# Kernel tuning notes

Measured on AMD Instinct MI355X. Metric: run time of the kernel, lower is better.

Reference implementation:

```python
import jax, jax.numpy as jnp
import numpy as np

TEMP = 0.1
LAM = 1.0
NORM_EPS = 1e-12   # torch F.normalize eps
COS_EPS = 1e-8     # torch F.cosine_similarity eps


def l2norm(x, axis):
    n = jnp.sqrt(jnp.sum(x * x, axis=axis, keepdims=True))
    return x / jnp.maximum(n, NORM_EPS)


def cos_sim(a, b, axis):
    na = jnp.sqrt(jnp.sum(a * a, axis=axis))
    nb = jnp.sqrt(jnp.sum(b * b, axis=axis))
    return jnp.sum(a * b, axis=axis) / jnp.maximum(na * nb, COS_EPS)


def setup_inputs() -> dict:
    key = jax.random.key(0)
    k1, k2, k3, k4, k5 = jax.random.split(key, 5)
    B, C, H, W = 32, 256, 32, 32
    return {
        "q_b": jax.random.normal(k1, (B, C, H, W), dtype=jnp.float32),
        "k_b": jax.random.normal(k2, (B, C, H, W), dtype=jnp.float32),
        "q_grid": jax.random.normal(k3, (B, C, H, W), dtype=jnp.float32),
        "k_grid": jax.random.normal(k4, (B, C, H, W), dtype=jnp.float32),
        "labels": jax.random.randint(k5, (B,), 0, 10, dtype=jnp.int64),
    }


def densecl(q_b, k_b, q_grid, k_grid, labels):
    B, C, H, W = q_b.shape
    S = H * W
    q_b = l2norm(q_b, axis=1)
    k_b = l2norm(k_b, axis=1)
    q_grid = l2norm(q_grid, axis=1)
    k_grid = l2norm(k_grid, axis=1)

    q_b_flat = q_b.reshape(B, C, S)
    k_b_flat = k_b.reshape(B, C, S)
    # spatial correspondence: [B, S, S]
    sim = jnp.einsum('bci,bcj->bij', q_b_flat, k_b_flat)
    max_sim_idx = jnp.argmax(sim, axis=-1)  # [B, S]

    Cg = q_grid.shape[1]
    q_grid_flat = q_grid.reshape(B, Cg, S)
    k_grid_flat = k_grid.reshape(B, Cg, S)
    idx = jnp.broadcast_to(max_sim_idx[:, None, :], (B, Cg, S))
    k_matched = jnp.take_along_axis(k_grid_flat, idx, axis=2)
    pos_sim = cos_sim(q_grid_flat, k_matched, axis=1) / TEMP  # [B, S]

    # random negative from a different-label sample (use_prototypes=False path)
    key = jax.random.key(42)
    u = jax.random.uniform(key, (B, B))
    mask = labels[:, None] != labels[None, :]
    neg_idx = jnp.argmax(jnp.where(mask, u, -1.0), axis=1)  # [B]
    neg_k = k_grid_flat[neg_idx]  # [B, Cg, S]
    neg_sim = cos_sim(q_grid_flat, neg_k, axis=1) / TEMP  # [B, S]

    loss = -jnp.log(jnp.exp(pos_sim) / (jnp.exp(pos_sim) + jnp.exp(neg_sim) + 1e-6))
    return jnp.mean(loss)


def reference(q_b, k_b, q_grid, k_grid, labels):
    return densecl(q_b, k_b, q_grid, k_grid, labels) * LAM
```

## Files before the change

kernel.cpp:

```cpp
#include <hip/hip_runtime.h>
#include <hip/hip_bf16.h>
#include <math.h>
#include <stdint.h>

#define BB 32
#define CC 256
#define SS 1024

typedef __attribute__((ext_vector_type(8))) short short8v;
typedef __attribute__((ext_vector_type(4))) float f32x4;

#define ASYNC16(g, l)                                                        \
  __builtin_amdgcn_global_load_lds(                                          \
      (const __attribute__((address_space(1))) void*)(g),                    \
      (__attribute__((address_space(3))) void*)(l), 16, 0, 0)

__device__ __forceinline__ unsigned short bf16_rne(float f) {
  unsigned int u = __float_as_uint(f);
  unsigned int r = (u + 0x7fffu + ((u >> 16) & 1u)) >> 16;
  return (unsigned short)r;
}

__device__ __forceinline__ void tf_round(uint32_t& x0, uint32_t& x1, int r) {
  x0 += x1;
  x1 = (x1 << r) | (x1 >> (32 - r));
  x1 ^= x0;
}

__device__ __forceinline__ void tf_gen(int t, float* u) {
  uint32_t x0 = (uint32_t)t;
  uint32_t x1 = (uint32_t)(t + 512);
  const uint32_t ks0 = 0u, ks1 = 42u, ks2 = 0x1BD11BDAu ^ 0u ^ 42u;
  x0 += ks0; x1 += ks1;
  tf_round(x0, x1, 13); tf_round(x0, x1, 15); tf_round(x0, x1, 26); tf_round(x0, x1, 6);
  x0 += ks1; x1 += ks2 + 1u;
  tf_round(x0, x1, 17); tf_round(x0, x1, 29); tf_round(x0, x1, 16); tf_round(x0, x1, 24);
  x0 += ks2; x1 += ks0 + 2u;
  tf_round(x0, x1, 13); tf_round(x0, x1, 15); tf_round(x0, x1, 26); tf_round(x0, x1, 6);
  x0 += ks0; x1 += ks1 + 3u;
  tf_round(x0, x1, 17); tf_round(x0, x1, 29); tf_round(x0, x1, 16); tf_round(x0, x1, 24);
  x0 += ks1; x1 += ks2 + 4u;
  tf_round(x0, x1, 13); tf_round(x0, x1, 15); tf_round(x0, x1, 26); tf_round(x0, x1, 6);
  x0 += ks2; x1 += ks0 + 5u;
  u[t]       = __uint_as_float((x0 >> 9) | 0x3f800000u) - 1.0f;
  u[t + 512] = __uint_as_float((x1 >> 9) | 0x3f800000u) - 1.0f;
}

__device__ __forceinline__ void tn_body(const float* __restrict__ src,
                                        unsigned short* __restrict__ dst,
                                        float* __restrict__ inv, int b, int s0,
                                        int tid, unsigned int* tile,
                                        float (*part)[65]) {
  const int sg = tid & 15;
  const int cq = tid >> 4;

  const float* sp = src + (size_t)b * CC * SS + s0 + sg * 4;
  float ssq[4] = {0.f, 0.f, 0.f, 0.f};

#pragma unroll
  for (int half = 0; half < 2; ++half) {
    float4 xa[4], xb[4];
#pragma unroll
    for (int kk = 0; kk < 4; ++kk) {
      int cp = cq + 16 * (half * 4 + kk);
      int c = cp * 2;
      xa[kk] = *(const float4*)(sp + ((size_t)c << 10));
      xb[kk] = *(const float4*)(sp + ((size_t)(c + 1) << 10));
    }
#pragma unroll
    for (int kk = 0; kk < 4; ++kk) {
      int cp = cq + 16 * (half * 4 + kk);
      float a[4] = {xa[kk].x, xa[kk].y, xa[kk].z, xa[kk].w};
      float bb[4] = {xb[kk].x, xb[kk].y, xb[kk].z, xb[kk].w};
#pragma unroll
      for (int e = 0; e < 4; ++e) {
        ssq[e] = fmaf(a[e], a[e], ssq[e]);
        ssq[e] = fmaf(bb[e], bb[e], ssq[e]);
        int r = sg * 4 + e;
        int colp = cp ^ (sg << 2);
        tile[r * 128 + colp] =
            (unsigned)bf16_rne(a[e]) | ((unsigned)bf16_rne(bb[e]) << 16);
      }
    }
  }
#pragma unroll
  for (int e = 0; e < 4; ++e) part[cq][sg * 4 + e] = ssq[e];
  __syncthreads();

  const int h = tid >> 5, cw = tid & 31;
  unsigned short* dp = dst + ((size_t)b * SS + s0) * CC;
#pragma unroll
  for (int p = 0; p < 8; ++p) {
    int r = p * 8 + h;
    int colb = (cw * 4) ^ ((r >> 2) << 2);
    uint4 pk = *(const uint4*)&tile[r * 128 + colb];
    *(uint4*)(dp + (size_t)r * CC + cw * 8) = pk;
  }
  if (tid < 64) {
    float s = 0.f;
#pragma unroll
    for (int k = 0; k < 16; ++k) s += part[k][tid];
    inv[b * SS + s0 + tid] = 1.0f / fmaxf(sqrtf(s), 1e-12f);
  }
}

__global__ __launch_bounds__(256, 4) void transnorm_kernel(
    const float* __restrict__ qb, const float* __restrict__ kb,
    unsigned short* __restrict__ qt, unsigned short* __restrict__ kt,
    float* __restrict__ invqb, float* __restrict__ invkb,
    const int* __restrict__ labels, int* __restrict__ negidx,
    unsigned long long* __restrict__ best, float* __restrict__ out) {
  const int bid = blockIdx.x;
  const int tid = threadIdx.x;

  __shared__ unsigned int tile[64 * 128];
  __shared__ float part[16][65];

  if (bid >= 1024) {
    if (bid == 1024) {
      float* u = (float*)&tile[0];
      tf_gen(tid, u);
      tf_gen(tid + 256, u);
      if (tid == 0) *out = 0.f;
      __syncthreads();
      if (tid < BB) {
        int lb = labels[tid];
        float bestv = -1.0f;
        int bj = 0;
        for (int j = 0; j < BB; ++j) {
          float v = (labels[j] != lb) ? u[tid * BB + j] : -1.0f;
          if (v > bestv) { bestv = v; bj = j; }
        }
        negidx[tid] = bj;
      }
    } else {
      unsigned long long* bp = best + (size_t)(bid - 1025) * 8192 + tid;
#pragma unroll
      for (int i = 0; i < 32; ++i) bp[(size_t)i * 256] = 0ull;
    }
    return;
  }

  const int which = bid >> 9;
  const int sub = bid & 511;
  tn_body(which ? kb : qb, which ? kt : qt, which ? invkb : invqb, sub >> 4,
          (sub & 15) * 64, tid, tile, part);
}

__device__ __forceinline__ void sim_stage(
    const unsigned short* __restrict__ aG, const unsigned short* __restrict__ bG,
    unsigned short* SA, unsigned short* SB, int ch, int w, int r8, int p) {
#pragma unroll
  for (int v = 0; v < 4; ++v) {
    int r = v * 32 + w * 8 + r8;
    int clog = p ^ (r & 7);
    ASYNC16(aG + (size_t)r * CC + ch * 64 + clog * 8, &SA[(v * 32 + w * 8) * 64]);
    ASYNC16(bG + (size_t)r * CC + ch * 64 + clog * 8, &SB[(v * 32 + w * 8) * 64]);
  }
}

__device__ __forceinline__ void sim_compute(
    const unsigned short* SA, const unsigned short* SB, f32x4 acc[4][4],
    int wi, int wj, int q4, int m16) {
#pragma unroll
  for (int kk = 0; kk < 2; ++kk) {
    short8v af[4], bf[4];
#pragma unroll
    for (int mt = 0; mt < 4; ++mt) {
      int i = wi + mt * 16 + m16;
      int cp = (kk * 4 + q4) ^ (i & 7);
      af[mt] = *(const short8v*)&SA[i * 64 + cp * 8];
      int j = wj + mt * 16 + m16;
      int cq = (kk * 4 + q4) ^ (j & 7);
      bf[mt] = *(const short8v*)&SB[j * 64 + cq * 8];
    }
#pragma unroll
    for (int mt = 0; mt < 4; ++mt)
#pragma unroll
      for (int nt = 0; nt < 4; ++nt)
        acc[mt][nt] = __builtin_amdgcn_mfma_f32_16x16x32_bf16(
            af[mt], bf[nt], acc[mt][nt], 0, 0, 0);
  }
}

__global__ __launch_bounds__(256, 2) void megasim_kernel(
    const unsigned short* __restrict__ qt, const unsigned short* __restrict__ kt,
    const float* __restrict__ invk, unsigned long long* __restrict__ best,
    const float* __restrict__ kg, unsigned short* __restrict__ kgt,
    float* __restrict__ invkg) {
  __shared__ __align__(16) char smem[68096];
  const int bid = blockIdx.x;
  const int t = threadIdx.x;

  if ((bid % 5) == 4) {
    const int tn_idx = bid / 5;
    tn_body(kg, kgt, invkg, tn_idx >> 4, (tn_idx & 15) * 64, t,
            (unsigned int*)smem, (float(*)[65])(smem + 32768));
    return;
  }

  const int x = bid & 7;
  const int k = ((bid % 40) - x) >> 3;
  int o = 0;
#pragma unroll
  for (int kk = 0; kk < 4; ++kk)
    if (kk < k && ((x + 8 * kk) % 5) != 4) ++o;
  const int W = x * 256 + (bid / 40) * 4 + o;
  const int b = W >> 6, it = (W >> 3) & 7, jt = W & 7;
  const int w = t >> 6, l = t & 63;

  unsigned short* sa0 = (unsigned short*)(smem);
  unsigned short* sa1 = (unsigned short*)(smem + 16384);
  unsigned short* sb0 = (unsigned short*)(smem + 32768);
  unsigned short* sb1 = (unsigned short*)(smem + 49152);
  unsigned long long (*cand2)[2] = (unsigned long long(*)[2])(smem + 65536);
  float* sinvk = (float*)(smem + 65536 + 2048);

  if (t < 128) sinvk[t] = invk[b * SS + jt * 128 + t];

  const unsigned short* aG = qt + ((size_t)b * SS + it * 128) * CC;
  const unsigned short* bG = kt + ((size_t)b * SS + jt * 128) * CC;

  f32x4 acc[4][4];
#pragma unroll
  for (int mt = 0; mt < 4; ++mt)
#pragma unroll
    for (int nt = 0; nt < 4; ++nt) acc[mt][nt] = (f32x4){0.f, 0.f, 0.f, 0.f};

  const int r8 = l >> 3, p = l & 7;
  const int q4 = l >> 4, m16 = l & 15;
  const int wi = (w >> 1) * 64, wj = (w & 1) * 64;

  sim_stage(aG, bG, sa0, sb0, 0, w, r8, p);
  __syncthreads();
  sim_stage(aG, bG, sa1, sb1, 1, w, r8, p);
  sim_compute(sa0, sb0, acc, wi, wj, q4, m16);
  __syncthreads();
  sim_stage(aG, bG, sa0, sb0, 2, w, r8, p);
  sim_compute(sa1, sb1, acc, wi, wj, q4, m16);
  __syncthreads();
  sim_stage(aG, bG, sa1, sb1, 3, w, r8, p);
  sim_compute(sa0, sb0, acc, wi, wj, q4, m16);
  __syncthreads();
  sim_compute(sa1, sb1, acc, wi, wj, q4, m16);

  float siv[4];
#pragma unroll
  for (int nt = 0; nt < 4; ++nt) siv[nt] = sinvk[wj + nt * 16 + m16];

  unsigned long long bp[4][4];
#pragma unroll
  for (int mt = 0; mt < 4; ++mt) {
#pragma unroll
    for (int e = 0; e < 4; ++e) {
      unsigned long long mx = 0ull;
#pragma unroll
      for (int nt = 0; nt < 4; ++nt) {
        float v = acc[mt][nt][e] * siv[nt];
        unsigned int u = __float_as_uint(v);
        u = (u & 0x80000000u) ? ~u : (u | 0x80000000u);
        int col = jt * 128 + wj + nt * 16 + m16;
        unsigned long long pk =
            ((unsigned long long)u << 32) | (unsigned)(1023 - col);
        mx = (pk > mx) ? pk : mx;
      }
      bp[mt][e] = mx;
    }
  }
#pragma unroll
  for (int d = 1; d < 16; d <<= 1) {
#pragma unroll
    for (int mt = 0; mt < 4; ++mt)
#pragma unroll
      for (int e = 0; e < 4; ++e) {
        unsigned long long o2 = __shfl_xor(bp[mt][e], d, 64);
        if (o2 > bp[mt][e]) bp[mt][e] = o2;
      }
  }
  if (m16 == 0) {
#pragma unroll
    for (int mt = 0; mt < 4; ++mt)
#pragma unroll
      for (int e = 0; e < 4; ++e)
        cand2[wi + mt * 16 + q4 * 4 + e][w & 1] = bp[mt][e];
  }
  __syncthreads();
  if (t < 128) {
    unsigned long long m0 = cand2[t][0], m1 = cand2[t][1];
    atomicMax(&best[b * SS + it * 128 + t], m0 > m1 ? m0 : m1);
  }
}

__global__ void negidx_kernel(const int* __restrict__ labels, int* __restrict__ negidx) {
  __shared__ float u[1024];
  int t = threadIdx.x;
  tf_gen(t, u);
  __syncthreads();
  if (t < BB) {
    int lb = labels[t];
    float bestv = -1.0f;
    int bj = 0;
    for (int j = 0; j < BB; ++j) {
      float v = (labels[j] != lb) ? u[t * BB + j] : -1.0f;
      if (v > bestv) { bestv = v; bj = j; }
    }
    negidx[t] = bj;
  }
}

__global__ __launch_bounds__(256) void loss_fused_kernel(
    const float* __restrict__ qg, const unsigned short* __restrict__ kgt,
    const float* __restrict__ invkg, const unsigned long long* __restrict__ best,
    const int* __restrict__ negidx, float* __restrict__ out) {
  const int tid = threadIdx.x;
  const int s_l = tid & 31, g = tid >> 5;
  const int P0 = blockIdx.x * 32;
  const int b = P0 >> 10;
  const int s = (P0 & (SS - 1)) + s_l;
  const int idx = b * SS + s;
  const int js = 1023 - (int)(best[idx] & 0xffffffffu);
  const int nb = negidx[b];

  const float* qcol = qg + ((size_t)b * CC + g * 32) * SS + s;
  const unsigned short* kp = kgt + ((size_t)b * SS + js) * CC + g * 32;
  const unsigned short* kn = kgt + ((size_t)nb * SS + s) * CC + g * 32;

  float dp = 0.f, dn = 0.f, sq = 0.f;
#pragma unroll
  for (int uu = 0; uu < 4; ++uu) {
    uint4 up = *(const uint4*)(kp + uu * 8);
    uint4 un = *(const uint4*)(kn + uu * 8);
    float q[8];
#pragma unroll
    for (int j = 0; j < 8; ++j) {
      q[j] = qcol[(size_t)(uu * 8 + j) << 10];
      sq = fmaf(q[j], q[j], sq);
    }
    float pv[8], nv[8];
    pv[0] = __uint_as_float(up.x << 16); pv[1] = __uint_as_float(up.x & 0xffff0000u);
    pv[2] = __uint_as_float(up.y << 16); pv[3] = __uint_as_float(up.y & 0xffff0000u);
    pv[4] = __uint_as_float(up.z << 16); pv[5] = __uint_as_float(up.z & 0xffff0000u);
    pv[6] = __uint_as_float(up.w << 16); pv[7] = __uint_as_float(up.w & 0xffff0000u);
    nv[0] = __uint_as_float(un.x << 16); nv[1] = __uint_as_float(un.x & 0xffff0000u);
    nv[2] = __uint_as_float(un.y << 16); nv[3] = __uint_as_float(un.y & 0xffff0000u);
    nv[4] = __uint_as_float(un.z << 16); nv[5] = __uint_as_float(un.z & 0xffff0000u);
    nv[6] = __uint_as_float(un.w << 16); nv[7] = __uint_as_float(un.w & 0xffff0000u);
#pragma unroll
    for (int j = 0; j < 8; ++j) {
      dp = fmaf(q[j], pv[j], dp);
      dn = fmaf(q[j], nv[j], dn);
    }
  }

  __shared__ float rdp[8][33], rdn[8][33], rsq[8][33];
  rdp[g][s_l] = dp;
  rdn[g][s_l] = dn;
  rsq[g][s_l] = sq;
  __syncthreads();
  if (tid < 32) {
    float DP = 0.f, DN = 0.f, SQ = 0.f;
#pragma unroll
    for (int k = 0; k < 8; ++k) {
      DP += rdp[k][tid];
      DN += rdn[k][tid];
      SQ += rsq[k][tid];
    }
    int s2 = (P0 & (SS - 1)) + tid;
    int idx2 = b * SS + s2;
    int js2 = 1023 - (int)(best[idx2] & 0xffffffffu);
    float iq = 1.0f / fmaxf(sqrtf(SQ), 1e-12f);
    float pvv = DP * iq * invkg[b * SS + js2] * 10.0f;
    float nvv = DN * iq * invkg[nb * SS + s2] * 10.0f;
    float elem = logf(expf(pvv) + expf(nvv) + 1e-6f) - pvv;
#pragma unroll
    for (int o = 16; o > 0; o >>= 1) elem += __shfl_down(elem, o, 32);
    if (tid == 0) atomicAdd(out, elem * (1.0f / (BB * SS)));
  }
}

__global__ __launch_bounds__(256) void norms_kernel(
    const float* __restrict__ qb, const float* __restrict__ kb,
    const float* __restrict__ qg, const float* __restrict__ kg,
    float* __restrict__ inv) {
  int t = blockIdx.x * 256 + threadIdx.x;
  int which = t >> 15;
  int bs = t & (BB * SS - 1);
  const float* src = (which == 0) ? qb : (which == 1) ? kb : (which == 2) ? qg : kg;
  int b = bs >> 10;
  int s = bs & (SS - 1);
  const float* p = src + (size_t)b * CC * SS + s;
  float ss = 0.f;
#pragma unroll 8
  for (int c = 0; c < CC; ++c) {
    float x = p[(size_t)c * SS];
    ss = fmaf(x, x, ss);
  }
  float n = fmaxf(sqrtf(ss), 1e-12f);
  inv[t] = 1.0f / n;
}

#define TI 64
#define TJ 128
#define KC 32

__global__ __launch_bounds__(256) void simargmax_kernel(
    const float* __restrict__ qb, const float* __restrict__ kb,
    const float* __restrict__ invq, const float* __restrict__ invk,
    int* __restrict__ amax) {
  const int b = blockIdx.x >> 4;
  const int i0 = (blockIdx.x & 15) * TI;
  const int t = threadIdx.x;
  const int ti = t >> 4;
  const int tj = t & 15;

  __shared__ float aQ[KC][TI];
  __shared__ float bK[KC][TJ];
  __shared__ float redv[TI][16];
  __shared__ int redj[TI][16];

  const float* qbase = qb + (size_t)b * CC * SS + i0;
  const float* kbase = kb + (size_t)b * CC * SS;
  const float* ivq = invq + b * SS + i0;
  const float* ivk = invk + b * SS;

  float best_v = -3.4e38f;
  int best_j = 0;

  for (int j0 = 0; j0 < SS; j0 += TJ) {
    float acc[4][8];
#pragma unroll
    for (int r = 0; r < 4; ++r)
#pragma unroll
      for (int rr = 0; rr < 8; ++rr) acc[r][rr] = 0.f;

    for (int c0 = 0; c0 < CC; c0 += KC) {
      __syncthreads();
#pragma unroll
      for (int v = 0; v < 2; ++v) {
        int f = t + v * 256;
        int cl = f >> 4;
        int sl = (f & 15) << 2;
        float4 qa = *(const float4*)(qbase + (size_t)(c0 + cl) * SS + sl);
        float4 iv = *(const float4*)(ivq + sl);
        aQ[cl][sl + 0] = qa.x * iv.x;
        aQ[cl][sl + 1] = qa.y * iv.y;
        aQ[cl][sl + 2] = qa.z * iv.z;
        aQ[cl][sl + 3] = qa.w * iv.w;
      }
#pragma unroll
      for (int v = 0; v < 4; ++v) {
        int f = t + v * 256;
        int cl = f >> 5;
        int sl = (f & 31) << 2;
        float4 ka = *(const float4*)(kbase + (size_t)(c0 + cl) * SS + j0 + sl);
        float4 ik = *(const float4*)(ivk + j0 + sl);
        bK[cl][sl + 0] = ka.x * ik.x;
        bK[cl][sl + 1] = ka.y * ik.y;
        bK[cl][sl + 2] = ka.z * ik.z;
        bK[cl][sl + 3] = ka.w * ik.w;
      }
      __syncthreads();
#pragma unroll
      for (int kc = 0; kc < KC; ++kc) {
        float4 a0 = *(const float4*)&aQ[kc][ti * 4];
        float4 b0 = *(const float4*)&bK[kc][tj * 8];
        float4 b1 = *(const float4*)&bK[kc][tj * 8 + 4];
        float av[4] = {a0.x, a0.y, a0.z, a0.w};
        float bv[8] = {b0.x, b0.y, b0.z, b0.w, b1.x, b1.y, b1.z, b1.w};
#pragma unroll
        for (int r = 0; r < 4; ++r)
#pragma unroll
          for (int rr = 0; rr < 8; ++rr)
            acc[r][rr] = fmaf(av[r], bv[rr], acc[r][rr]);
      }
    }
    __syncthreads();
#pragma unroll
    for (int r = 0; r < 4; ++r) {
      float v = acc[r][0];
      int jb = j0 + tj * 8;
#pragma unroll
      for (int rr = 1; rr < 8; ++rr) {
        if (acc[r][rr] > v) { v = acc[r][rr]; jb = j0 + tj * 8 + rr; }
      }
      redv[ti * 4 + r][tj] = v;
      redj[ti * 4 + r][tj] = jb;
    }
    __syncthreads();
    if (t < TI) {
#pragma unroll
      for (int ww = 0; ww < 16; ++ww) {
        float v = redv[t][ww];
        if (v > best_v) { best_v = v; best_j = redj[t][ww]; }
      }
    }
  }
  if (t < TI) amax[b * SS + i0 + t] = best_j;
}

__global__ __launch_bounds__(256) void loss_kernel(
    const float* __restrict__ qg, const float* __restrict__ kg,
    const float* __restrict__ invq, const float* __restrict__ invk,
    const int* __restrict__ amax, const int* __restrict__ negidx,
    float* __restrict__ out) {
  int t = blockIdx.x * 256 + threadIdx.x;
  int b = t >> 10;
  int s = t & (SS - 1);
  int js = amax[t];
  int nb = negidx[b];
  const float* qcol = qg + (size_t)b * CC * SS + s;
  const float* kpcol = kg + (size_t)b * CC * SS + js;
  const float* kncol = kg + (size_t)nb * CC * SS + s;
  float dp = 0.f, dn = 0.f;
#pragma unroll 8
  for (int c = 0; c < CC; ++c) {
    float q = qcol[(size_t)c * SS];
    dp = fmaf(q, kpcol[(size_t)c * SS], dp);
    dn = fmaf(q, kncol[(size_t)c * SS], dn);
  }
  float iq = invq[t];
  float pv = dp * iq * invk[b * SS + js] * 10.0f;
  float nv = dn * iq * invk[nb * SS + s] * 10.0f;
  float elem = logf(expf(pv) + expf(nv) + 1e-6f) - pv;

  __shared__ float red[256];
  red[threadIdx.x] = elem;
  __syncthreads();
  for (int o = 128; o > 0; o >>= 1) {
    if (threadIdx.x < o) red[threadIdx.x] += red[threadIdx.x + o];
    __syncthreads();
  }
  if (threadIdx.x == 0) atomicAdd(out, red[0] * (1.0f / (BB * SS)));
}

extern "C" void kernel_launch(void* const* d_in, const int* in_sizes, int n_in,
                              void* d_out, int out_size, void* d_ws, size_t ws_size,
                              hipStream_t stream) {
  const float* qb = (const float*)d_in[0];
  const float* kb = (const float*)d_in[1];
  const float* qg = (const float*)d_in[2];
  const float* kg = (const float*)d_in[3];
  const int* labels = (const int*)d_in[4];

  char* ws = (char*)d_ws;
  float* invqb = (float*)ws;
  float* invkb = (float*)(ws + 128 * 1024);
  float* invkg = (float*)(ws + 256 * 1024);
  unsigned long long* best = (unsigned long long*)(ws + 384 * 1024);
  int* negidx = (int*)(ws + 640 * 1024);
  unsigned short* qt = (unsigned short*)(ws + (1 << 20));
  unsigned short* kt = (unsigned short*)(ws + (17 << 20));
  unsigned short* kgt = (unsigned short*)(ws + (33 << 20));

  const size_t need = (size_t)49 * 1024 * 1024;
  const bool fast = ws_size >= need;

  if (fast) {
    transnorm_kernel<<<1029, 256, 0, stream>>>(qb, kb, qt, kt, invqb, invkb,
                                               labels, negidx, best,
                                               (float*)d_out);
    megasim_kernel<<<2560, 256, 0, stream>>>(qt, kt, invkb, best, kg, kgt,
                                             invkg);
    loss_fused_kernel<<<1024, 256, 0, stream>>>(qg, kgt, invkg, best, negidx,
                                                (float*)d_out);
  } else {
    hipMemsetAsync(d_out, 0, sizeof(float), stream);
    float* inv = (float*)ws;
    int* amax = (int*)(ws + 512 * 1024);
    int* negidx2 = (int*)(ws + 640 * 1024);
    norms_kernel<<<(4 * BB * SS) / 256, 256, 0, stream>>>(qb, kb, qg, kg, inv);
    simargmax_kernel<<<BB * (SS / TI), 256, 0, stream>>>(
        qb, kb, inv + 0 * BB * SS, inv + 1 * BB * SS, amax);
    negidx_kernel<<<1, 512, 0, stream>>>(labels, negidx2);
    loss_kernel<<<(BB * SS) / 256, 256, 0, stream>>>(
        qg, kg, inv + 2 * BB * SS, inv + 3 * BB * SS, amax, negidx2,
        (float*)d_out);
  }
}
```

Baseline: 201.0 us.

## Load MFMA operands directly from global memory instead of staging through LDS

Measured after the change: 235.9 us. +17.4%, slower.

```diff
diff --git a/kernel.cpp b/kernel.cpp
--- a/kernel.cpp
+++ b/kernel.cpp
@@ -9,11 +9,6 @@
 
 typedef __attribute__((ext_vector_type(8))) short short8v;
 typedef __attribute__((ext_vector_type(4))) float f32x4;
-
-#define ASYNC16(g, l)                                                        \
-  __builtin_amdgcn_global_load_lds(                                          \
-      (const __attribute__((address_space(1))) void*)(g),                    \
-      (__attribute__((address_space(3))) void*)(l), 16, 0, 0)
 
 __device__ __forceinline__ unsigned short bf16_rne(float f) {
   unsigned int u = __float_as_uint(f);
@@ -147,48 +142,12 @@
           (sub & 15) * 64, tid, tile, part);
 }
 
-__device__ __forceinline__ void sim_stage(
-    const unsigned short* __restrict__ aG, const unsigned short* __restrict__ bG,
-    unsigned short* SA, unsigned short* SB, int ch, int w, int r8, int p) {
-#pragma unroll
-  for (int v = 0; v < 4; ++v) {
-    int r = v * 32 + w * 8 + r8;
-    int clog = p ^ (r & 7);
-    ASYNC16(aG + (size_t)r * CC + ch * 64 + clog * 8, &SA[(v * 32 + w * 8) * 64]);
-    ASYNC16(bG + (size_t)r * CC + ch * 64 + clog * 8, &SB[(v * 32 + w * 8) * 64]);
-  }
-}
-
-__device__ __forceinline__ void sim_compute(
-    const unsigned short* SA, const unsigned short* SB, f32x4 acc[4][4],
-    int wi, int wj, int q4, int m16) {
-#pragma unroll
-  for (int kk = 0; kk < 2; ++kk) {
-    short8v af[4], bf[4];
-#pragma unroll
-    for (int mt = 0; mt < 4; ++mt) {
-      int i = wi + mt * 16 + m16;
-      int cp = (kk * 4 + q4) ^ (i & 7);
-      af[mt] = *(const short8v*)&SA[i * 64 + cp * 8];
-      int j = wj + mt * 16 + m16;
-      int cq = (kk * 4 + q4) ^ (j & 7);
-      bf[mt] = *(const short8v*)&SB[j * 64 + cq * 8];
-    }
-#pragma unroll
-    for (int mt = 0; mt < 4; ++mt)
-#pragma unroll
-      for (int nt = 0; nt < 4; ++nt)
-        acc[mt][nt] = __builtin_amdgcn_mfma_f32_16x16x32_bf16(
-            af[mt], bf[nt], acc[mt][nt], 0, 0, 0);
-  }
-}
-
-__global__ __launch_bounds__(256, 2) void megasim_kernel(
+__global__ __launch_bounds__(256, 4) void megasim_kernel(
     const unsigned short* __restrict__ qt, const unsigned short* __restrict__ kt,
     const float* __restrict__ invk, unsigned long long* __restrict__ best,
     const float* __restrict__ kg, unsigned short* __restrict__ kgt,
     float* __restrict__ invkg) {
-  __shared__ __align__(16) char smem[68096];
+  __shared__ __align__(16) char smem[36928];
   const int bid = blockIdx.x;
   const int t = threadIdx.x;
 
@@ -209,44 +168,42 @@
   const int b = W >> 6, it = (W >> 3) & 7, jt = W & 7;
   const int w = t >> 6, l = t & 63;
 
-  unsigned short* sa0 = (unsigned short*)(smem);
-  unsigned short* sa1 = (unsigned short*)(smem + 16384);
-  unsigned short* sb0 = (unsigned short*)(smem + 32768);
-  unsigned short* sb1 = (unsigned short*)(smem + 49152);
-  unsigned long long (*cand2)[2] = (unsigned long long(*)[2])(smem + 65536);
-  float* sinvk = (float*)(smem + 65536 + 2048);
-
-  if (t < 128) sinvk[t] = invk[b * SS + jt * 128 + t];
-
-  const unsigned short* aG = qt + ((size_t)b * SS + it * 128) * CC;
-  const unsigned short* bG = kt + ((size_t)b * SS + jt * 128) * CC;
-
-  f32x4 acc[4][4];
-#pragma unroll
-  for (int mt = 0; mt < 4; ++mt)
-#pragma unroll
-    for (int nt = 0; nt < 4; ++nt) acc[mt][nt] = (f32x4){0.f, 0.f, 0.f, 0.f};
-
-  const int r8 = l >> 3, p = l & 7;
+  unsigned long long (*cand2)[2] = (unsigned long long(*)[2])(smem);
+
   const int q4 = l >> 4, m16 = l & 15;
   const int wi = (w >> 1) * 64, wj = (w & 1) * 64;
 
-  sim_stage(aG, bG, sa0, sb0, 0, w, r8, p);
-  __syncthreads();
-  sim_stage(aG, bG, sa1, sb1, 1, w, r8, p);
-  sim_compute(sa0, sb0, acc, wi, wj, q4, m16);
-  __syncthreads();
-  sim_stage(aG, bG, sa0, sb0, 2, w, r8, p);
-  sim_compute(sa1, sb1, acc, wi, wj, q4, m16);
-  __syncthreads();
-  sim_stage(aG, bG, sa1, sb1, 3, w, r8, p);
-  sim_compute(sa0, sb0, acc, wi, wj, q4, m16);
-  __syncthreads();
-  sim_compute(sa1, sb1, acc, wi, wj, q4, m16);
+  const unsigned short* aP =
+      qt + ((size_t)b * SS + it * 128 + wi + m16) * CC + q4 * 8;
+  const unsigned short* bP =
+      kt + ((size_t)b * SS + jt * 128 + wj + m16) * CC + q4 * 8;
+
+  f32x4 acc[4][4];
+#pragma unroll
+  for (int mt = 0; mt < 4; ++mt)
+#pragma unroll
+    for (int nt = 0; nt < 4; ++nt) acc[mt][nt] = (f32x4){0.f, 0.f, 0.f, 0.f};
+
+#pragma unroll
+  for (int kk = 0; kk < 8; ++kk) {
+    short8v af[4], bf[4];
+#pragma unroll
+    for (int mt = 0; mt < 4; ++mt) {
+      af[mt] = *(const short8v*)(aP + (size_t)mt * 16 * CC + kk * 32);
+      bf[mt] = *(const short8v*)(bP + (size_t)mt * 16 * CC + kk * 32);
+    }
+#pragma unroll
+    for (int mt = 0; mt < 4; ++mt)
+#pragma unroll
+      for (int nt = 0; nt < 4; ++nt)
+        acc[mt][nt] = __builtin_amdgcn_mfma_f32_16x16x32_bf16(
+            af[mt], bf[nt], acc[mt][nt], 0, 0, 0);
+  }
 
   float siv[4];
 #pragma unroll
-  for (int nt = 0; nt < 4; ++nt) siv[nt] = sinvk[wj + nt * 16 + m16];
+  for (int nt = 0; nt < 4; ++nt)
+    siv[nt] = invk[b * SS + jt * 128 + wj + nt * 16 + m16];
 
   unsigned long long bp[4][4];
 #pragma unroll
```
